# Optimization experiments

Hardware: AMD Instinct MI355X
Metric: run time of the kernel (lower is better)

Reference implementation:

```python
import jax, jax.numpy as jnp
import numpy as np
import math
from itertools import combinations_with_replacement

BN_EPS = 1e-5


def _gen_exponents(d, degree):
    num_poly = math.comb(degree + d, d)
    exps = np.zeros((num_poly, d), dtype=np.int32)
    i = 0
    for total_degree in range(degree + 1):
        for combo in combinations_with_replacement(range(d), total_degree):
            for var in combo:
                exps[i, var] += 1
            i += 1
    return exps[1:]  # drop the constant (all-zero) multi-index


def setup_inputs() -> dict:
    key = jax.random.key(0)
    ks = jax.random.split(key, 12)
    d, degree = 3, 15
    B, N = 32, 2048
    exponents = jnp.asarray(_gen_exponents(d, degree))  # (M=815, 3) int32
    M = exponents.shape[0]
    # points in (-0.9, 0.9) so acos and its gradient are well-defined
    x = (jax.random.uniform(ks[0], (B, d, N), dtype=jnp.float32) * 1.8 - 0.9)

    def lin(k, din, dout):
        kw, kb = jax.random.split(k)
        scale = 1.0 / np.sqrt(din)
        W = jax.random.uniform(kw, (din, dout), jnp.float32, -scale, scale)
        b = jax.random.uniform(kb, (dout,), jnp.float32, -scale, scale)
        return W, b

    dims = [M, 512, 256, 128]
    inp = {"x": x, "exponents": exponents}
    for i in range(3):
        W, b = lin(ks[1 + i], dims[i], dims[i + 1])
        h = dims[i + 1]
        inp[f"W{i+1}"], inp[f"b{i+1}"] = W, b
        inp[f"g{i+1}"] = jnp.ones((h,), jnp.float32)   # BN weight
        inp[f"be{i+1}"] = jnp.zeros((h,), jnp.float32)  # BN bias
        inp[f"rm{i+1}"] = jnp.zeros((h,), jnp.float32)  # BN running mean
        inp[f"rv{i+1}"] = jnp.ones((h,), jnp.float32)   # BN running var
    W4, b4 = lin(ks[10], 128, 40)
    inp["W4"], inp["b4"] = W4, b4
    return inp


def _moments_chebyshev(x, exponents):
    # x: (B, d, N) -> X: (B, N, d)
    X = jnp.transpose(x, (0, 2, 1))
    ac = jnp.arccos(X)                              # (B, N, d)
    e = exponents.astype(ac.dtype)                  # (M, d)
    # T_{e_j}(X_j) = cos(e_j * acos(X_j)); product over d, mean over N
    cheb = jnp.cos(e[None, None, :, :] * ac[:, :, None, :])  # (B, N, M, d)
    return cheb.prod(axis=-1).sum(axis=1) / X.shape[1]       # (B, M)


def _lin_bn_relu(h, W, b, g, be, rm, rv):
    h = h @ W + b
    h = g * (h - rm) / jnp.sqrt(rv + BN_EPS) + be  # BatchNorm1d, eval mode
    return jax.nn.relu(h)


def reference(x, exponents,
              W1, b1, g1, be1, rm1, rv1,
              W2, b2, g2, be2, rm2, rv2,
              W3, b3, g3, be3, rm3, rv3,
              W4, b4):
    feats = _moments_chebyshev(x, exponents)  # (B, 815)
    h = _lin_bn_relu(feats, W1, b1, g1, be1, rm1, rv1)
    h = _lin_bn_relu(h, W2, b2, g2, be2, rm2, rv2)
    h = _lin_bn_relu(h, W3, b3, g3, be3, rm3, rv3)
    return h @ W4 + b4  # (B, 40)
```

## Files before the change

### kernel.cpp

```cpp
#include <hip/hip_runtime.h>
#include <math.h>

#define NPTS   2048
#define BATCH  32
#define M_POLY 815
#define GPB    2
#define NSPLIT 16
#define QSTR   160
#define T0OFF  10240
#define BN_EPS 1e-5f

__device__ __forceinline__ bool decode_chunk(int ci, int& Lo, int& k0o, int& co, int& qo) {
    int idx = 0, qoff = 0;
    for (int l = 0; l < 16; ++l) {
        const int nb   = (l + 4) >> 2;
        const int cmin = (l == 0) ? 1 : 0;
        const int nc   = 16 - l - cmin;
        for (int kb = 0; kb < nb; ++kb) {
            if (ci < idx + nc) {
                Lo = l; k0o = kb * 4; co = cmin + (ci - idx);
                qo = qoff + kb * 4;
                return true;
            }
            idx += nc;
        }
        qoff += nb * 4;
    }
    return false;
}

__global__ __launch_bounds__(256) void moments_kernel(
    const float* __restrict__ x,
    float*       __restrict__ part)
{
    __shared__ __align__(16) float P[64 * QSTR + 1024];
    const int t  = threadIdx.x;
    const int sb = blockIdx.x;
    const int b  = blockIdx.y;
    const int nn = t & 63;
    const int qq = t >> 6;
    const int sw = 4 * (nn & 7);
    const int base = nn * QSTR;

    int L, k0, c, qoff4;
    decode_chunk(t, L, k0, c, qoff4);
    const bool dual = (t >= 253);
    const int k02   = dual ? 4 * (t - 252) : 4;
    const int qoff42 = 144 + k02;

    int qx[8], q2x[8];
    #pragma unroll
    for (int r = 0; r < 8; ++r) {
        qx[r]  = qoff4  ^ (4 * r);
        q2x[r] = qoff42 ^ (4 * r);
    }

    float a[4]  = {0.f, 0.f, 0.f, 0.f};
    float a2[4] = {0.f, 0.f, 0.f, 0.f};
    const float* xb = x + (size_t)b * 3 * NPTS;

    for (int g = 0; g < GPB; ++g) {
        if (g) __syncthreads();
        {
            const int n = (sb * GPB + g) * 64 + nn;
            const float x1 = xb[NPTS + n], x2 = xb[2 * NPTS + n];
            float T1r[16], T2r[16];
            T1r[0] = 1.f; T1r[1] = x1;
            #pragma unroll
            for (int k = 2; k < 16; ++k) T1r[k] = 2.f * x1 * T1r[k-1] - T1r[k-2];
            T2r[0] = 1.f; T2r[1] = x2;
            #pragma unroll
            for (int k = 2; k < 16; ++k) T2r[k] = 2.f * x2 * T2r[k-1] - T2r[k-2];

            #define QVAL(SS,E) (((E) <= (SS)) ? T1r[((SS)-(E)) & 15] * T2r[(E) & 15] : 0.f)
            #define ROWQ(SS, QO) { \
                _Pragma("unroll") \
                for (int blk2 = 0; blk2 < ((SS)+4)/4; ++blk2) { \
                    float4 v; \
                    v.x = QVAL(SS, 4*blk2+0); v.y = QVAL(SS, 4*blk2+1); \
                    v.z = QVAL(SS, 4*blk2+2); v.w = QVAL(SS, 4*blk2+3); \
                    *(float4*)&P[base + (((QO) + 4*blk2) ^ sw)] = v; } }

            if (qq == 0) {
                const float x0 = xb[n];
                float T0r[16];
                T0r[0] = 1.f; T0r[1] = x0;
                #pragma unroll
                for (int k = 2; k < 16; ++k) T0r[k] = 2.f * x0 * T0r[k-1] - T0r[k-2];
                #pragma unroll
                for (int cc = 0; cc < 16; ++cc)
                    P[T0OFF + cc * 64 + ((nn + 4 * cc) & 63)] = T0r[cc];
                ROWQ(0, 0)  ROWQ(1, 4)  ROWQ(2, 8)  ROWQ(3, 12)
            } else if (qq == 1) {
                ROWQ(4, 16) ROWQ(5, 24) ROWQ(6, 32) ROWQ(7, 40) ROWQ(8, 48)
            } else if (qq == 2) {
                ROWQ(9, 60) ROWQ(10, 72) ROWQ(11, 84) ROWQ(12, 96)
            } else {
                ROWQ(13, 112) ROWQ(14, 128) ROWQ(15, 144)
            }
            #undef ROWQ
            #undef QVAL
        }
        __syncthreads();

        #pragma unroll 4
        for (int q4 = 0; q4 < 16; ++q4) {
            const int np0 = q4 * 4;
            const float4 t0q =
                *(const float4*)&P[T0OFF + c * 64 + ((np0 + 4 * c) & 63)];
            #pragma unroll
            for (int i = 0; i < 4; ++i) {
                const int np = np0 + i;
                const float* rp = &P[np * QSTR];
                const float  t0v = ((const float*)&t0q)[i];
                const float4 qv = *(const float4*)&rp[qx[np & 7]];
                a[0] = fmaf(t0v, qv.x, a[0]);
                a[1] = fmaf(t0v, qv.y, a[1]);
                a[2] = fmaf(t0v, qv.z, a[2]);
                a[3] = fmaf(t0v, qv.w, a[3]);
                if (dual) {
                    const float4 p2 = *(const float4*)&rp[q2x[np & 7]];
                    a2[0] += p2.x; a2[1] += p2.y; a2[2] += p2.z; a2[3] += p2.w;
                }
            }
        }
    }

    float* pb = part + ((size_t)b * NSPLIT + sb) * M_POLY;
    {
        const int D  = c + L;
        const int mb = D * (D + 1) * (D + 2) / 6 - 1 + L * (L + 1) / 2;
        const int nv = (L - k0 + 1 < 4) ? (L - k0 + 1) : 4;
        #pragma unroll
        for (int i = 0; i < 4; ++i)
            if (i < nv) pb[mb + k0 + i] = a[i];
    }
    if (dual) {
        const int mb = 799;
        #pragma unroll
        for (int i = 0; i < 4; ++i)
            pb[mb + k02 + i] = a2[i];
    }
}

__global__ __launch_bounds__(512) void l1_kernel(
    const float* __restrict__ part,
    const float* __restrict__ W1, const float* __restrict__ b1,
    const float* __restrict__ g1, const float* __restrict__ be1,
    const float* __restrict__ rm1, const float* __restrict__ rv1,
    float* __restrict__ h1)
{
    __shared__ float fs[816];
    __shared__ float red[8][64];
    const int t  = threadIdx.x;
    const int og = blockIdx.x;
    const int b  = blockIdx.y;

    {
        float s0 = 0.f;
        #pragma unroll
        for (int sp = 0; sp < NSPLIT; ++sp)
            s0 += part[((size_t)b * NSPLIT + sp) * M_POLY + t];
        fs[t] = s0 * (1.0f / (float)NPTS);
        if (t < 303) {
            float s1 = 0.f;
            #pragma unroll
            for (int sp = 0; sp < NSPLIT; ++sp)
                s1 += part[((size_t)b * NSPLIT + sp) * M_POLY + 512 + t];
            fs[512 + t] = s1 * (1.0f / (float)NPTS);
        }
        if (t == 0) fs[815] = 0.f;
    }
    __syncthreads();

    const int o  = og * 64 + (t & 63);
    const int cg = t >> 6;
    const int kb = cg * 102;
    float acc = 0.f;
    #pragma unroll 6
    for (int kk = 0; kk < 102; ++kk) {
        const int k  = kb + kk;
        const int kr = (k < 815) ? k : 814;
        acc = fmaf(fs[k], W1[(size_t)kr * 512 + o], acc);
    }
    red[cg][t & 63] = acc;
    __syncthreads();

    if (t < 64) {
        float dot = 0.f;
        #pragma unroll
        for (int j = 0; j < 8; ++j) dot += red[j][t];
        const int oo = og * 64 + t;
        const float v = (dot + b1[oo] - rm1[oo]) * g1[oo] * rsqrtf(rv1[oo] + BN_EPS) + be1[oo];
        h1[b * 512 + oo] = v > 0.f ? v : 0.f;
    }
}

__global__ __launch_bounds__(512) void l2_kernel(
    const float* __restrict__ h1,
    const float* __restrict__ W2, const float* __restrict__ b2,
    const float* __restrict__ g2, const float* __restrict__ be2,
    const float* __restrict__ rm2, const float* __restrict__ rv2,
    float* __restrict__ h2)
{
    __shared__ float hs[512];
    __shared__ float red[16][32];
    const int t  = threadIdx.x;
    const int og = blockIdx.x;
    const int b  = blockIdx.y;

    hs[t] = h1[b * 512 + t];
    __syncthreads();

    const int o  = og * 32 + (t & 31);
    const int cg = t >> 5;
    const int kb = cg * 32;
    float acc = 0.f;
    #pragma unroll
    for (int kk = 0; kk < 32; ++kk)
        acc = fmaf(hs[kb + kk], W2[(size_t)(kb + kk) * 256 + o], acc);
    red[cg][t & 31] = acc;
    __syncthreads();

    if (t < 32) {
        float dot = 0.f;
        #pragma unroll
        for (int j = 0; j < 16; ++j) dot += red[j][t];
        const int oo = og * 32 + t;
        const float v = (dot + b2[oo] - rm2[oo]) * g2[oo] * rsqrtf(rv2[oo] + BN_EPS) + be2[oo];
        h2[b * 256 + oo] = v > 0.f ? v : 0.f;
    }
}

__global__ __launch_bounds__(512) void l34_kernel(
    const float* __restrict__ h2,
    const float* __restrict__ W3, const float* __restrict__ b3,
    const float* __restrict__ g3, const float* __restrict__ be3,
    const float* __restrict__ rm3, const float* __restrict__ rv3,
    const float* __restrict__ W4, const float* __restrict__ b4,
    float* __restrict__ out)
{
    __shared__ float hs[256];
    __shared__ float red3[4][128];
    __shared__ float h3s[128];
    __shared__ float red4[8][64];
    const int t = threadIdx.x;
    const int b = blockIdx.x;

    if (t < 256) hs[t] = h2[b * 256 + t];
    __syncthreads();

    {
        const int o  = t & 127;
        const int cg = t >> 7;
        const int kb = cg * 64;
        float acc = 0.f;
        #pragma unroll 8
        for (int kk = 0; kk < 64; ++kk)
            acc = fmaf(hs[kb + kk], W3[(size_t)(kb + kk) * 128 + o], acc);
        red3[cg][o] = acc;
    }
    __syncthreads();
    if (t < 128) {
        const float dot = red3[0][t] + red3[1][t] + red3[2][t] + red3[3][t];
        const float v = (dot + b3[t] - rm3[t]) * g3[t] * rsqrtf(rv3[t] + BN_EPS) + be3[t];
        h3s[t] = v > 0.f ? v : 0.f;
    }
    __syncthreads();

    {
        const int o  = t & 63;
        const int om = (o < 40) ? o : 39;
        const int cg = t >> 6;
        const int kb = cg * 16;
        float acc = 0.f;
        #pragma unroll
        for (int kk = 0; kk < 16; ++kk)
            acc = fmaf(h3s[kb + kk], W4[(size_t)(kb + kk) * 40 + om], acc);
        red4[cg][o] = acc;
    }
    __syncthreads();
    if (t < 40) {
        float dot = 0.f;
        #pragma unroll
        for (int j = 0; j < 8; ++j) dot += red4[j][t];
        out[b * 40 + t] = dot + b4[t];
    }
}

extern "C" void kernel_launch(void* const* d_in, const int* in_sizes, int n_in,
                              void* d_out, int out_size, void* d_ws, size_t ws_size,
                              hipStream_t stream) {
    const float* x  = (const float*)d_in[0];
    const float* W1 = (const float*)d_in[2];
    const float* b1 = (const float*)d_in[3];
    const float* g1 = (const float*)d_in[4];
    const float* be1= (const float*)d_in[5];
    const float* rm1= (const float*)d_in[6];
    const float* rv1= (const float*)d_in[7];
    const float* W2 = (const float*)d_in[8];
    const float* b2 = (const float*)d_in[9];
    const float* g2 = (const float*)d_in[10];
    const float* be2= (const float*)d_in[11];
    const float* rm2= (const float*)d_in[12];
    const float* rv2= (const float*)d_in[13];
    const float* W3 = (const float*)d_in[14];
    const float* b3 = (const float*)d_in[15];
    const float* g3 = (const float*)d_in[16];
    const float* be3= (const float*)d_in[17];
    const float* rm3= (const float*)d_in[18];
    const float* rv3= (const float*)d_in[19];
    const float* W4 = (const float*)d_in[20];
    const float* b4 = (const float*)d_in[21];
    float* out = (float*)d_out;

    float* part = (float*)d_ws;
    float* h1   = part + (size_t)BATCH * NSPLIT * M_POLY;
    float* h2   = h1 + (size_t)BATCH * 512;

    moments_kernel<<<dim3(NSPLIT, BATCH), 256, 0, stream>>>(x, part);
    l1_kernel<<<dim3(8, BATCH), 512, 0, stream>>>(part,
        W1, b1, g1, be1, rm1, rv1, h1);
    l2_kernel<<<dim3(8, BATCH), 512, 0, stream>>>(h1,
        W2, b2, g2, be2, rm2, rv2, h2);
    l34_kernel<<<BATCH, 512, 0, stream>>>(h2,
        W3, b3, g3, be3, rm3, rv3, W4, b4, out);
}
```

Measured before the change: 32.04 us.

## Split moments point loop across two thread halves; batch-pair L1 blocks

The moments kernel now runs 512 threads per block. Table generation is spread over eight 64-thread groups instead of four, and each half of the block accumulates over half of the 64 points per group. The two halves' partial sums are then combined through shared memory before the global write. The L1 kernel now handles two batch rows per block, so each W1 load is reused for two dot products and the grid is halved. The cost is an extra shared-memory reduction with barriers, higher register and LDS pressure per block, and fewer L1 blocks in flight.

```diff
diff --git a/kernel.cpp b/kernel.cpp
--- a/kernel.cpp
+++ b/kernel.cpp
@@ -3,11 +3,12 @@
 
 #define NPTS   2048
 #define BATCH  32
-#define M_POLY 815
 #define GPB    2
 #define NSPLIT 16
+#define M_POLY 815
 #define QSTR   160
 #define T0OFF  10240
+#define SCROFF 11264
 #define BN_EPS 1e-5f
 
 __device__ __forceinline__ bool decode_chunk(int ci, int& Lo, int& k0o, int& co, int& qo) {
@@ -29,23 +30,25 @@
     return false;
 }
 
-__global__ __launch_bounds__(256) void moments_kernel(
+__global__ __launch_bounds__(512) void moments_kernel(
     const float* __restrict__ x,
     float*       __restrict__ part)
 {
-    __shared__ __align__(16) float P[64 * QSTR + 1024];
+    __shared__ __align__(16) float P[12304];
     const int t  = threadIdx.x;
     const int sb = blockIdx.x;
     const int b  = blockIdx.y;
+    const int tt = t & 255;
+    const int hh = t >> 8;
     const int nn = t & 63;
     const int qq = t >> 6;
     const int sw = 4 * (nn & 7);
     const int base = nn * QSTR;
 
     int L, k0, c, qoff4;
-    decode_chunk(t, L, k0, c, qoff4);
-    const bool dual = (t >= 253);
-    const int k02   = dual ? 4 * (t - 252) : 4;
+    decode_chunk(tt, L, k0, c, qoff4);
+    const bool dual = (tt >= 253);
+    const int k02   = dual ? 4 * (tt - 252) : 4;
     const int qoff42 = 144 + k02;
 
     int qx[8], q2x[8];
@@ -90,13 +93,21 @@
                 #pragma unroll
                 for (int cc = 0; cc < 16; ++cc)
                     P[T0OFF + cc * 64 + ((nn + 4 * cc) & 63)] = T0r[cc];
-                ROWQ(0, 0)  ROWQ(1, 4)  ROWQ(2, 8)  ROWQ(3, 12)
+                ROWQ(0, 0)
             } else if (qq == 1) {
-                ROWQ(4, 16) ROWQ(5, 24) ROWQ(6, 32) ROWQ(7, 40) ROWQ(8, 48)
+                ROWQ(1, 4)   ROWQ(2, 8)   ROWQ(3, 12)
             } else if (qq == 2) {
-                ROWQ(9, 60) ROWQ(10, 72) ROWQ(11, 84) ROWQ(12, 96)
+                ROWQ(4, 16)  ROWQ(5, 24)
+            } else if (qq == 3) {
+                ROWQ(6, 32)  ROWQ(7, 40)
+            } else if (qq == 4) {
+                ROWQ(8, 48)  ROWQ(9, 60)
+            } else if (qq == 5) {
+                ROWQ(10, 72) ROWQ(11, 84)
+            } else if (qq == 6) {
+                ROWQ(12, 96) ROWQ(13, 112)
             } else {
-                ROWQ(13, 112) ROWQ(14, 128) ROWQ(15, 144)
+                ROWQ(14, 128) ROWQ(15, 144)
             }
             #undef ROWQ
             #undef QVAL
@@ -104,8 +115,8 @@
         __syncthreads();
 
         #pragma unroll 4
-        for (int q4 = 0; q4 < 16; ++q4) {
-            const int np0 = q4 * 4;
+        for (int q4 = 0; q4 < 8; ++q4) {
+            const int np0 = hh * 32 + q4 * 4;
             const float4 t0q =
                 *(const float4*)&P[T0OFF + c * 64 + ((np0 + 4 * c) & 63)];
             #pragma unroll
@@ -126,20 +137,32 @@
         }
     }
 
-    float* pb = part + ((size_t)b * NSPLIT + sb) * M_POLY;
-    {
-        const int D  = c + L;
-        const int mb = D * (D + 1) * (D + 2) / 6 - 1 + L * (L + 1) / 2;
-        const int nv = (L - k0 + 1 < 4) ? (L - k0 + 1) : 4;
-        #pragma unroll
-        for (int i = 0; i < 4; ++i)
-            if (i < nv) pb[mb + k0 + i] = a[i];
-    }
-    if (dual) {
-        const int mb = 799;
-        #pragma unroll
-        for (int i = 0; i < 4; ++i)
-            pb[mb + k02 + i] = a2[i];
+    __syncthreads();
+    if (hh == 1) {
+        #pragma unroll
+        for (int i = 0; i < 4; ++i) P[SCROFF + tt * 4 + i] = a[i];
+        if (dual) {
+            #pragma unroll
+            for (int i = 0; i < 4; ++i) P[SCROFF + 1024 + (tt - 253) * 4 + i] = a2[i];
+        }
+    }
+    __syncthreads();
+    if (hh == 0) {
+        float* pb = part + ((size_t)b * NSPLIT + sb) * M_POLY;
+        {
+            const int D  = c + L;
+            const int mb = D * (D + 1) * (D + 2) / 6 - 1 + L * (L + 1) / 2;
+            const int nv = (L - k0 + 1 < 4) ? (L - k0 + 1) : 4;
+            #pragma unroll
+            for (int i = 0; i < 4; ++i)
+                if (i < nv) pb[mb + k0 + i] = a[i] + P[SCROFF + tt * 4 + i];
+        }
+        if (dual) {
+            const int mb = 799;
+            #pragma unroll
+            for (int i = 0; i < 4; ++i)
+                pb[mb + k02 + i] = a2[i] + P[SCROFF + 1024 + (tt - 253) * 4 + i];
+        }
     }
 }
 
@@ -150,49 +173,62 @@
     const float* __restrict__ rm1, const float* __restrict__ rv1,
     float* __restrict__ h1)
 {
-    __shared__ float fs[816];
-    __shared__ float red[8][64];
+    __shared__ float fs0[816], fs1[816];
+    __shared__ float red[8][64][2];
     const int t  = threadIdx.x;
     const int og = blockIdx.x;
-    const int b  = blockIdx.y;
+    const int b0 = blockIdx.y * 2;
+    const int b1i = b0 + 1;
 
     {
-        float s0 = 0.f;
-        #pragma unroll
-        for (int sp = 0; sp < NSPLIT; ++sp)
-            s0 += part[((size_t)b * NSPLIT + sp) * M_POLY + t];
-        fs[t] = s0 * (1.0f / (float)NPTS);
+        float s0 = 0.f, s1 = 0.f;
+        #pragma unroll
+        for (int sp = 0; sp < NSPLIT; ++sp) {
+            s0 += part[((size_t)b0 * NSPLIT + sp) * M_POLY + t];
+            s1 += part[((size_t)b1i * NSPLIT + sp) * M_POLY + t];
+        }
+        fs0[t] = s0 * (1.0f / (float)NPTS);
+        fs1[t] = s1 * (1.0f / (float)NPTS);
         if (t < 303) {
-            float s1 = 0.f;
-            #pragma unroll
-            for (int sp = 0; sp < NSPLIT; ++sp)
-                s1 += part[((size_t)b * NSPLIT + sp) * M_POLY + 512 + t];
-            fs[512 + t] = s1 * (1.0f / (float)NPTS);
-        }
-        if (t == 0) fs[815] = 0.f;
+            float u0 = 0.f, u1 = 0.f;
+            #pragma unroll
+            for (int sp = 0; sp < NSPLIT; ++sp) {
+                u0 += part[((size_t)b0 * NSPLIT + sp) * M_POLY + 512 + t];
+                u1 += part[((size_t)b1i * NSPLIT + sp) * M_POLY + 512 + t];
+            }
+            fs0[512 + t] = u0 * (1.0f / (float)NPTS);
+            fs1[512 + t] = u1 * (1.0f / (float)NPTS);
+        }
+        if (t == 0) { fs0[815] = 0.f; fs1[815] = 0.f; }
     }
     __syncthreads();
 
     const int o  = og * 64 + (t & 63);
     const int cg = t >> 6;
     const int kb = cg * 102;
-    float acc = 0.f;
+    float acc0 = 0.f, acc1 = 0.f;
     #pragma unroll 6
     for (int kk = 0; kk < 102; ++kk) {
         const int k  = kb + kk;
         const int kr = (k < 815) ? k : 814;
-        acc = fmaf(fs[k], W1[(size_t)kr * 512 + o], acc);
-    }
-    red[cg][t & 63] = acc;
-    __syncthreads();
-
-    if (t < 64) {
+        const float w = W1[(size_t)kr * 512 + o];
+        acc0 = fmaf(fs0[k], w, acc0);
+        acc1 = fmaf(fs1[k], w, acc1);
+    }
+    red[cg][t & 63][0] = acc0;
+    red[cg][t & 63][1] = acc1;
+    __syncthreads();
+
+    if (t < 128) {
+        const int lane  = t & 63;
+        const int which = t >> 6;
         float dot = 0.f;
         #pragma unroll
-        for (int j = 0; j < 8; ++j) dot += red[j][t];
-        const int oo = og * 64 + t;
+        for (int j = 0; j < 8; ++j) dot += red[j][lane][which];
+        const int oo = og * 64 + lane;
+        const int bb = b0 + which;
         const float v = (dot + b1[oo] - rm1[oo]) * g1[oo] * rsqrtf(rv1[oo] + BN_EPS) + be1[oo];
-        h1[b * 512 + oo] = v > 0.f ? v : 0.f;
+        h1[bb * 512 + oo] = v > 0.f ? v : 0.f;
     }
 }
 
@@ -318,8 +354,8 @@
     float* h1   = part + (size_t)BATCH * NSPLIT * M_POLY;
     float* h2   = h1 + (size_t)BATCH * 512;
 
-    moments_kernel<<<dim3(NSPLIT, BATCH), 256, 0, stream>>>(x, part);
-    l1_kernel<<<dim3(8, BATCH), 512, 0, stream>>>(part,
+    moments_kernel<<<dim3(NSPLIT, BATCH), 512, 0, stream>>>(x, part);
+    l1_kernel<<<dim3(8, BATCH / 2), 512, 0, stream>>>(part,
         W1, b1, g1, be1, rm1, rv1, h1);
     l2_kernel<<<dim3(8, BATCH), 512, 0, stream>>>(h1,
         W2, b2, g2, be2, rm2, rv2, h2);
```

Measured after the change: 34.91 us. +9.0%, slower.
